# Optimization experiments

Hardware: AMD Instinct MI355X
Metric: run time of the kernel (lower is better)

## Reference

```python
import jax, jax.numpy as jnp
import numpy as np

NUM_USERS = 100000
NUM_ITEMS = 50000
EMBED_DIM = 128
NNZ = 2000000
N_LAYERS = 3


def setup_inputs() -> dict:
    key = jax.random.key(0)
    k1, k2, k3, k4, k5 = jax.random.split(key, 5)
    stdv = 1.0 / np.sqrt(EMBED_DIM)
    user_pref = jax.random.uniform(k1, (NUM_USERS, EMBED_DIM), jnp.float32, -stdv, stdv)
    item_pref = jax.random.uniform(k2, (NUM_ITEMS, EMBED_DIM), jnp.float32, -stdv, stdv)
    vals = jax.random.uniform(k3, (NNZ,), jnp.float32)
    rows = jax.random.randint(k4, (NNZ,), 0, NUM_USERS, jnp.int32)
    cols = jax.random.randint(k5, (NNZ,), 0, NUM_ITEMS, jnp.int32)
    return {"user_pref": user_pref, "item_pref": item_pref, "vals": vals,
            "rows": rows, "cols": cols}


def _spmm(vals, src_idx, dst_idx, x, num_out):
    # y[dst] += vals * x[src]  — SpMM over COO edge list
    msgs = vals[:, None] * x[src_idx]            # [nnz, D]
    return jax.ops.segment_sum(msgs, dst_idx, num_segments=num_out)


def reference(user_pref, item_pref, vals, rows, cols):
    u, it = user_pref, item_pref
    u_sum, i_sum = user_pref, item_pref
    for _ in range(N_LAYERS):
        # u_next = Graph @ item_layer ; i_next = Graph.T @ user_layer (same layer index)
        u_next = _spmm(vals, cols, rows, it, NUM_USERS)   # [U, D]
        i_next = _spmm(vals, rows, cols, u, NUM_ITEMS)    # [I, D]
        u, it = u_next, i_next
        u_sum = u_sum + u
        i_sum = i_sum + it
    inv = 1.0 / (N_LAYERS + 1)
    return (u_sum * inv, i_sum * inv)
```

## Files before the change

kernel.cpp:

```cpp
#include <hip/hip_runtime.h>


#define NUM_USERS 100000
#define NUM_ITEMS 50000
#define EMBED_DIM 128
#define NNZ_COUNT 2000000
#define NBUCK_U 391
#define NBUCK_I 196
#define EPB 8192
#define NBLK 245


__device__ __forceinline__ unsigned bf16_rnd(float f) {
    unsigned u = __float_as_uint(f);
    return (u + 0x7FFFu + ((u >> 16) & 1u)) >> 16;
}
__device__ __forceinline__ unsigned pack_bf16(float x, float y) {
    return bf16_rnd(x) | (bf16_rnd(y) << 16);
}

__global__ __launch_bounds__(256) void to_bf16_kernel(
    const float* __restrict__ a, unsigned* __restrict__ o, int n8)
{
    int i = blockIdx.x * 256 + threadIdx.x;
    if (i >= n8) return;
    const float4* a4 = reinterpret_cast<const float4*>(a);
    float4 x = a4[i * 2], y = a4[i * 2 + 1];
    uint4 r;
    r.x = pack_bf16(x.x, x.y); r.y = pack_bf16(x.z, x.w);
    r.z = pack_bf16(y.x, y.y); r.w = pack_bf16(y.z, y.w);
    reinterpret_cast<uint4*>(o)[i] = r;
}


__global__ __launch_bounds__(256) void msplit_hist(
    const int* __restrict__ rows, const int* __restrict__ cols,
    int* __restrict__ hist_u, int* __restrict__ hist_i)
{
    __shared__ int h[NBUCK_U + NBUCK_I];
    for (int i = threadIdx.x; i < NBUCK_U + NBUCK_I; i += 256) h[i] = 0;
    __syncthreads();
    const int base = blockIdx.x * EPB;
    const int end = min(base + EPB, NNZ_COUNT);
    for (int e = base + threadIdx.x; e < end; e += 256) {
        atomicAdd(&h[rows[e] >> 8], 1);
        atomicAdd(&h[NBUCK_U + (cols[e] >> 8)], 1);
    }
    __syncthreads();
    for (int b = threadIdx.x; b < NBUCK_U; b += 256)
        hist_u[b * NBLK + blockIdx.x] = h[b];
    for (int b = threadIdx.x; b < NBUCK_I; b += 256)
        hist_i[b * NBLK + blockIdx.x] = h[NBUCK_U + b];
}

__global__ __launch_bounds__(256) void msplit_offsets(
    const int* __restrict__ hist_u, const int* __restrict__ hist_i,
    int* __restrict__ offs_u, int* __restrict__ offs_i,
    int* __restrict__ tot_u, int* __restrict__ tot_i)
{
    __shared__ int buf[256];
    int b = blockIdx.x;
    const int* hist; int* offs; int* tot; int nbuck;
    if (b < NBUCK_U) { hist = hist_u; offs = offs_u; tot = tot_u; nbuck = NBUCK_U; }
    else { b -= NBUCK_U; hist = hist_i; offs = offs_i; tot = tot_i; nbuck = NBUCK_I; }
    const int t = threadIdx.x;
    const int x = (t < NBLK) ? hist[b * NBLK + t] : 0;
    buf[t] = x;
    __syncthreads();
    for (int d = 1; d < 256; d <<= 1) {
        const int y = (t >= d) ? buf[t - d] : 0;
        __syncthreads();
        buf[t] += y;
        __syncthreads();
    }
    if (t < NBLK) offs[t * nbuck + b] = buf[t] - x;
    if (t == 255) tot[b] = buf[255];
}

__global__ __launch_bounds__(512) void scan_buckets(
    const int* __restrict__ tot_u, int* __restrict__ bbase_u,
    const int* __restrict__ tot_i, int* __restrict__ bbase_i)
{
    __shared__ int buf[512];
    const int t = threadIdx.x;
    const int* tot; int* bbase; int nb;
    if (blockIdx.x == 0) { tot = tot_u; bbase = bbase_u; nb = NBUCK_U; }
    else                 { tot = tot_i; bbase = bbase_i; nb = NBUCK_I; }
    const int v = (t < nb) ? tot[t] : 0;
    buf[t] = v;
    __syncthreads();
    for (int d = 1; d < 512; d <<= 1) {
        const int y = (t >= d) ? buf[t - d] : 0;
        __syncthreads();
        buf[t] += y;
        __syncthreads();
    }
    if (t <= nb) bbase[t] = buf[t] - v;
}

__global__ __launch_bounds__(256) void msplit_scatter(
    const int* __restrict__ rows, const int* __restrict__ cols,
    const float* __restrict__ vals,
    const int* __restrict__ offs_u, const int* __restrict__ offs_i,
    const int* __restrict__ bbase_u, const int* __restrict__ bbase_i,
    int2* __restrict__ stage_u, int2* __restrict__ stage_i)
{
    __shared__ int cu[NBUCK_U];
    __shared__ int ci[NBUCK_I];
    const int t = threadIdx.x;
    for (int b = t; b < NBUCK_U; b += 256)
        cu[b] = offs_u[blockIdx.x * NBUCK_U + b] + bbase_u[b];
    for (int b = t; b < NBUCK_I; b += 256)
        ci[b] = offs_i[blockIdx.x * NBUCK_I + b] + bbase_i[b];
    __syncthreads();
    const int base = blockIdx.x * EPB;
    const int end = min(base + EPB, NNZ_COUNT);
    for (int e = base + t; e < end; e += 256) {
        const int r = rows[e];
        const int c = cols[e];
        const int vb = __float_as_int(vals[e]);
        const int su = atomicAdd(&cu[r >> 8], 1);
        stage_u[su] = make_int2(c | ((r & 255) << 16), vb);
        const int si = atomicAdd(&ci[c >> 8], 1);
        stage_i[si] = make_int2(r | ((c & 255) << 17), vb);
    }
}

__global__ __launch_bounds__(256) void bucket_build(
    const int* __restrict__ bbase_u, const int2* __restrict__ stage_u,
    int2* __restrict__ pairs_u, int* __restrict__ ptr_u,
    const int* __restrict__ bbase_i, const int2* __restrict__ stage_i,
    int2* __restrict__ pairs_i, int* __restrict__ ptr_i)
{
    __shared__ int hcnt[256];
    __shared__ int buf[256];
    __shared__ int cur[256];
    const int t = threadIdx.x;
    int b = blockIdx.x;
    const bool uside = (b < NBUCK_U);
    const int* bbase; const int2* stage; int2* pairs; int* ptr; int n; int sh;
    if (uside) { bbase = bbase_u; stage = stage_u; pairs = pairs_u; ptr = ptr_u; n = NUM_USERS; sh = 16; }
    else { b -= NBUCK_U; bbase = bbase_i; stage = stage_i; pairs = pairs_i; ptr = ptr_i; n = NUM_ITEMS; sh = 17; }
    const int beg = bbase[b];
    const int end = bbase[b + 1];

    hcnt[t] = 0;
    __syncthreads();
    for (int idx = beg + t; idx < end; idx += 256)
        atomicAdd(&hcnt[(stage[idx].x >> sh) & 255], 1);
    __syncthreads();

    const int v = hcnt[t];
    buf[t] = v;
    __syncthreads();
    for (int d = 1; d < 256; d <<= 1) {
        const int y = (t >= d) ? buf[t - d] : 0;
        __syncthreads();
        buf[t] += y;
        __syncthreads();
    }
    const int rowbase = beg + buf[t] - v;
    cur[t] = rowbase;
    const int first = b << 8;
    if (first + t < n) ptr[first + t] = rowbase;
    if (first + t == n) ptr[n] = end;
    else if (first + 256 == n && t == 0) ptr[n] = end;
    __syncthreads();

    for (int idx = beg + t; idx < end; idx += 256) {
        const int2 s = stage[idx];
        const int local   = (s.x >> sh) & 255;
        const int payload = uside ? (s.x & 0xFFFF) : (s.x & 0x1FFFF);
        const int slot = atomicAdd(&cur[local], 1);
        pairs[slot] = make_int2(payload, s.y);
    }
}


template<bool WRITE_DST, bool HAS_BASE>
__device__ __forceinline__ void spmm_row_bf(
    const int* __restrict__ ptr, const int2* __restrict__ pairs,
    const unsigned* __restrict__ src, unsigned* __restrict__ dst,
    float* __restrict__ sum, const float* __restrict__ base,
    int row, int lane, float scale)
{
    const int start = ptr[row];
    const int end   = ptr[row + 1];
    float2 acc = make_float2(0.f, 0.f);

    for (int chunk = start; chunk < end; chunk += 64) {
        const int idx = chunk + lane;
        int2 p = make_int2(0, 0);
        if (idx < end) p = pairs[idx];
        int m = end - chunk; if (m > 64) m = 64;

        int j = 0;
        for (; j + 4 <= m; j += 4) {
            const int   c0 = __shfl(p.x, j),     c1 = __shfl(p.x, j + 1);
            const int   c2 = __shfl(p.x, j + 2), c3 = __shfl(p.x, j + 3);
            const float v0 = __int_as_float(__shfl(p.y, j));
            const float v1 = __int_as_float(__shfl(p.y, j + 1));
            const float v2 = __int_as_float(__shfl(p.y, j + 2));
            const float v3 = __int_as_float(__shfl(p.y, j + 3));
            const unsigned g0 = src[(size_t)c0 * 64 + lane];
            const unsigned g1 = src[(size_t)c1 * 64 + lane];
            const unsigned g2 = src[(size_t)c2 * 64 + lane];
            const unsigned g3 = src[(size_t)c3 * 64 + lane];
            acc.x += v0 * __uint_as_float(g0 << 16);
            acc.y += v0 * __uint_as_float(g0 & 0xFFFF0000u);
            acc.x += v1 * __uint_as_float(g1 << 16);
            acc.y += v1 * __uint_as_float(g1 & 0xFFFF0000u);
            acc.x += v2 * __uint_as_float(g2 << 16);
            acc.y += v2 * __uint_as_float(g2 & 0xFFFF0000u);
            acc.x += v3 * __uint_as_float(g3 << 16);
            acc.y += v3 * __uint_as_float(g3 & 0xFFFF0000u);
        }
        for (; j < m; ++j) {
            const int   c = __shfl(p.x, j);
            const float v = __int_as_float(__shfl(p.y, j));
            const unsigned g = src[(size_t)c * 64 + lane];
            acc.x += v * __uint_as_float(g << 16);
            acc.y += v * __uint_as_float(g & 0xFFFF0000u);
        }
    }

    if (WRITE_DST) dst[(size_t)row * 64 + lane] = pack_bf16(acc.x, acc.y);

    const size_t o = (size_t)row * EMBED_DIM + (lane << 1);
    float2 bsv;
    if (HAS_BASE) bsv = *reinterpret_cast<const float2*>(base + o);
    else          bsv = *reinterpret_cast<const float2*>(sum + o);
    bsv.x = (bsv.x + acc.x) * scale;
    bsv.y = (bsv.y + acc.y) * scale;
    *reinterpret_cast<float2*>(sum + o) = bsv;
}

template<bool WRITE_DST, bool HAS_BASE>
__global__ __launch_bounds__(256) void csr_spmm_dual_bf(
    const int*  __restrict__ ptr_u, const int2* __restrict__ pairs_u,
    const unsigned* __restrict__ src_u, unsigned* __restrict__ dst_u,
    float* __restrict__ sum_u, const float* __restrict__ base_u,
    const int*  __restrict__ ptr_i, const int2* __restrict__ pairs_i,
    const unsigned* __restrict__ src_i, unsigned* __restrict__ dst_i,
    float* __restrict__ sum_i, const float* __restrict__ base_i,
    int GU, float scale)
{
    const int lane = threadIdx.x & 63;
    const int w = threadIdx.x >> 6;
    if ((int)blockIdx.x < GU) {
        const int row = blockIdx.x * 4 + w;
        if (row < NUM_USERS)
            spmm_row_bf<WRITE_DST, HAS_BASE>(ptr_u, pairs_u, src_u, dst_u, sum_u, base_u, row, lane, scale);
    } else {
        const int row = ((int)blockIdx.x - GU) * 4 + w;
        if (row < NUM_ITEMS)
            spmm_row_bf<WRITE_DST, HAS_BASE>(ptr_i, pairs_i, src_i, dst_i, sum_i, base_i, row, lane, scale);
    }
}


__global__ __launch_bounds__(256) void edge_spmm(
    const float* __restrict__ vals, const int* __restrict__ rows,
    const int* __restrict__ cols, const float* __restrict__ u_src,
    const float* __restrict__ i_src, float* __restrict__ u_dst,
    float* __restrict__ i_dst, int nnz)
{
    const int lane = threadIdx.x & 31;
    const int e = blockIdx.x * 8 + (threadIdx.x >> 5);
    if (e >= nnz) return;
    const float v = vals[e];
    const size_t ro = (size_t)rows[e] * EMBED_DIM + lane * 4;
    const size_t co = (size_t)cols[e] * EMBED_DIM + lane * 4;
    const float4 iv = *reinterpret_cast<const float4*>(i_src + co);
    const float4 uv = *reinterpret_cast<const float4*>(u_src + ro);
    atomicAdd(u_dst + ro + 0, v * iv.x); atomicAdd(u_dst + ro + 1, v * iv.y);
    atomicAdd(u_dst + ro + 2, v * iv.z); atomicAdd(u_dst + ro + 3, v * iv.w);
    atomicAdd(i_dst + co + 0, v * uv.x); atomicAdd(i_dst + co + 1, v * uv.y);
    atomicAdd(i_dst + co + 2, v * uv.z); atomicAdd(i_dst + co + 3, v * uv.w);
}

__global__ __launch_bounds__(256) void acc_scale(
    float* __restrict__ out, const float* __restrict__ x, long n, float scale)
{
    long i = ((long)blockIdx.x * blockDim.x + threadIdx.x) * 4;
    if (i >= n) return;
    float4 o = *reinterpret_cast<float4*>(out + i);
    float4 a = *reinterpret_cast<const float4*>(x + i);
    o.x = (o.x + a.x) * scale; o.y = (o.y + a.y) * scale;
    o.z = (o.z + a.z) * scale; o.w = (o.w + a.w) * scale;
    *reinterpret_cast<float4*>(out + i) = o;
}


extern "C" void kernel_launch(void* const* d_in, const int* in_sizes, int n_in,
                              void* d_out, int out_size, void* d_ws, size_t ws_size,
                              hipStream_t stream)
{
    const float* user = (const float*)d_in[0];
    const float* item = (const float*)d_in[1];
    const float* vals = (const float*)d_in[2];
    const int*   rows = (const int*)d_in[3];
    const int*   cols = (const int*)d_in[4];

    const size_t UD = (size_t)NUM_USERS * EMBED_DIM;
    const size_t ID = (size_t)NUM_ITEMS * EMBED_DIM;

    float* out_u = (float*)d_out;
    float* out_i = out_u + UD;

    char* ws = (char*)d_ws;
    unsigned* user_bf = (unsigned*)ws;              ws += UD * 2;
    unsigned* item_bf = (unsigned*)ws;              ws += ID * 2;
    unsigned* uA = (unsigned*)ws;                   ws += UD * 2;
    unsigned* uB = (unsigned*)ws;                   ws += UD * 2;
    unsigned* iA = (unsigned*)ws;                   ws += ID * 2;
    unsigned* iB = (unsigned*)ws;                   ws += ID * 2;
    int2* pairs_u = (int2*)ws;                      ws += (size_t)NNZ_COUNT * 8;
    int2* pairs_i = (int2*)ws;                      ws += (size_t)NNZ_COUNT * 8;
    int2* stage_u = (int2*)ws;                      ws += (size_t)NNZ_COUNT * 8;
    int2* stage_i = (int2*)ws;                      ws += (size_t)NNZ_COUNT * 8;
    int* ptr_u = (int*)ws;                          ws += (NUM_USERS + 1) * 4;
    int* ptr_i = (int*)ws;                          ws += (NUM_ITEMS + 1) * 4;
    int* bbase_u = (int*)ws;                        ws += (NBUCK_U + 1) * 4;
    int* bbase_i = (int*)ws;                        ws += (NBUCK_I + 1) * 4;
    const size_t REQ = (size_t)(ws - (char*)d_ws);

    int* hist_u = (int*)pairs_u;
    int* hist_i = hist_u + NBUCK_U * NBLK;
    int* offs_u = hist_i + NBUCK_I * NBLK;
    int* offs_i = offs_u + NBLK * NBUCK_U;
    int* tot_u  = offs_i + NBLK * NBUCK_I;
    int* tot_i  = tot_u + NBUCK_U;

    if (ws_size >= REQ) {
        to_bf16_kernel<<<(int)(UD / 8 / 256), 256, 0, stream>>>(user, user_bf, (int)(UD / 8));
        to_bf16_kernel<<<(int)(ID / 8 / 256), 256, 0, stream>>>(item, item_bf, (int)(ID / 8));

        msplit_hist<<<NBLK, 256, 0, stream>>>(rows, cols, hist_u, hist_i);
        msplit_offsets<<<NBUCK_U + NBUCK_I, 256, 0, stream>>>(
            hist_u, hist_i, offs_u, offs_i, tot_u, tot_i);
        scan_buckets<<<2, 512, 0, stream>>>(tot_u, bbase_u, tot_i, bbase_i);
        msplit_scatter<<<NBLK, 256, 0, stream>>>(
            rows, cols, vals, offs_u, offs_i, bbase_u, bbase_i, stage_u, stage_i);
        bucket_build<<<NBUCK_U + NBUCK_I, 256, 0, stream>>>(
            bbase_u, stage_u, pairs_u, ptr_u,
            bbase_i, stage_i, pairs_i, ptr_i);

        const int GU = (NUM_USERS + 3) / 4;
        const int GI = (NUM_ITEMS + 3) / 4;

        csr_spmm_dual_bf<true, true><<<GU + GI, 256, 0, stream>>>(
            ptr_u, pairs_u, item_bf, uA, out_u, user,
            ptr_i, pairs_i, user_bf, iA, out_i, item, GU, 1.0f);
        csr_spmm_dual_bf<true, false><<<GU + GI, 256, 0, stream>>>(
            ptr_u, pairs_u, iA, uB, out_u, nullptr,
            ptr_i, pairs_i, uA, iB, out_i, nullptr, GU, 1.0f);
        csr_spmm_dual_bf<false, false><<<GU + GI, 256, 0, stream>>>(
            ptr_u, pairs_u, iB, uA, out_u, nullptr,
            ptr_i, pairs_i, uB, iA, out_i, nullptr, GU, 0.25f);
    } else {
        char* fw = (char*)d_ws;
        float* fuA = (float*)fw;                    fw += UD * 4;
        float* fuB = (float*)fw;                    fw += UD * 4;
        float* fiA = (float*)fw;                    fw += ID * 4;
        float* fiB = (float*)fw;                    fw += ID * 4;

        const int EDGE_BLOCKS = (NNZ_COUNT + 7) / 8;
        const int ACC_U = (int)(UD / 1024), ACC_I = (int)(ID / 1024);

        hipMemcpyAsync(out_u, user, UD * 4, hipMemcpyDeviceToDevice, stream);
        hipMemcpyAsync(out_i, item, ID * 4, hipMemcpyDeviceToDevice, stream);

        hipMemsetAsync(fuA, 0, UD * 4, stream);
        hipMemsetAsync(fiA, 0, ID * 4, stream);
        edge_spmm<<<EDGE_BLOCKS, 256, 0, stream>>>(vals, rows, cols, user, item, fuA, fiA, NNZ_COUNT);
        acc_scale<<<ACC_U, 256, 0, stream>>>(out_u, fuA, (long)UD, 1.0f);
        acc_scale<<<ACC_I, 256, 0, stream>>>(out_i, fiA, (long)ID, 1.0f);

        hipMemsetAsync(fuB, 0, UD * 4, stream);
        hipMemsetAsync(fiB, 0, ID * 4, stream);
        edge_spmm<<<EDGE_BLOCKS, 256, 0, stream>>>(vals, rows, cols, fuA, fiA, fuB, fiB, NNZ_COUNT);
        acc_scale<<<ACC_U, 256, 0, stream>>>(out_u, fuB, (long)UD, 1.0f);
        acc_scale<<<ACC_I, 256, 0, stream>>>(out_i, fiB, (long)ID, 1.0f);

        hipMemsetAsync(fuA, 0, UD * 4, stream);
        hipMemsetAsync(fiA, 0, ID * 4, stream);
        edge_spmm<<<EDGE_BLOCKS, 256, 0, stream>>>(vals, rows, cols, fuB, fiB, fuA, fiA, NNZ_COUNT);
        acc_scale<<<ACC_U, 256, 0, stream>>>(out_u, fuA, (long)UD, 0.25f);
        acc_scale<<<ACC_I, 256, 0, stream>>>(out_i, fiA, (long)ID, 0.25f);
    }
}
```

Before: 704.2 us.

## Pack CSR pairs into 32-bit words and defer layer-sum accumulation to final pass

```diff
diff --git a/kernel.cpp b/kernel.cpp
--- a/kernel.cpp
+++ b/kernel.cpp
@@ -19,17 +19,26 @@
     return bf16_rnd(x) | (bf16_rnd(y) << 16);
 }
 
-__global__ __launch_bounds__(256) void to_bf16_kernel(
-    const float* __restrict__ a, unsigned* __restrict__ o, int n8)
+__global__ __launch_bounds__(256) void to_bf16_dual(
+    const float* __restrict__ a, unsigned* __restrict__ oa, int na8,
+    const float* __restrict__ b, unsigned* __restrict__ ob, int nb8)
 {
     int i = blockIdx.x * 256 + threadIdx.x;
-    if (i >= n8) return;
-    const float4* a4 = reinterpret_cast<const float4*>(a);
-    float4 x = a4[i * 2], y = a4[i * 2 + 1];
+    const float4* s4; uint4* d4;
+    if (i < na8) {
+        s4 = reinterpret_cast<const float4*>(a) + i * 2;
+        d4 = reinterpret_cast<uint4*>(oa) + i;
+    } else {
+        i -= na8;
+        if (i >= nb8) return;
+        s4 = reinterpret_cast<const float4*>(b) + i * 2;
+        d4 = reinterpret_cast<uint4*>(ob) + i;
+    }
+    float4 x = s4[0], y = s4[1];
     uint4 r;
     r.x = pack_bf16(x.x, x.y); r.y = pack_bf16(x.z, x.w);
     r.z = pack_bf16(y.x, y.y); r.w = pack_bf16(y.z, y.w);
-    reinterpret_cast<uint4*>(o)[i] = r;
+    *d4 = r;
 }
 
 
@@ -128,9 +137,9 @@
 
 __global__ __launch_bounds__(256) void bucket_build(
     const int* __restrict__ bbase_u, const int2* __restrict__ stage_u,
-    int2* __restrict__ pairs_u, int* __restrict__ ptr_u,
+    unsigned* __restrict__ pairs_u, int* __restrict__ ptr_u,
     const int* __restrict__ bbase_i, const int2* __restrict__ stage_i,
-    int2* __restrict__ pairs_i, int* __restrict__ ptr_i)
+    unsigned* __restrict__ pairs_i, int* __restrict__ ptr_i)
 {
     __shared__ int hcnt[256];
     __shared__ int buf[256];
@@ -138,7 +147,7 @@
     const int t = threadIdx.x;
     int b = blockIdx.x;
     const bool uside = (b < NBUCK_U);
-    const int* bbase; const int2* stage; int2* pairs; int* ptr; int n; int sh;
+    const int* bbase; const int2* stage; unsigned* pairs; int* ptr; int n; int sh;
     if (uside) { bbase = bbase_u; stage = stage_u; pairs = pairs_u; ptr = ptr_u; n = NUM_USERS; sh = 16; }
     else { b -= NBUCK_U; bbase = bbase_i; stage = stage_i; pairs = pairs_i; ptr = ptr_i; n = NUM_ITEMS; sh = 17; }
     const int beg = bbase[b];
@@ -169,20 +178,30 @@
 
     for (int idx = beg + t; idx < end; idx += 256) {
         const int2 s = stage[idx];
-        const int local   = (s.x >> sh) & 255;
-        const int payload = uside ? (s.x & 0xFFFF) : (s.x & 0x1FFFF);
+        const int local = (s.x >> sh) & 255;
+        const unsigned vb = bf16_rnd(__int_as_float(s.y));
+        unsigned packed;
+        if (uside) packed = (unsigned)(s.x & 0xFFFF) | (vb << 16);
+        else       packed = (unsigned)(s.x & 0x1FFFF) | ((vb & 0x7FFFu) << 17);
         const int slot = atomicAdd(&cur[local], 1);
-        pairs[slot] = make_int2(payload, s.y);
-    }
-}
-
-
-template<bool WRITE_DST, bool HAS_BASE>
+        pairs[slot] = packed;
+    }
+}
+
+
+template<bool USIDE>
+__device__ __forceinline__ void decode_pair(unsigned s, int& c, float& v) {
+    if (USIDE) { c = (int)(s & 0xFFFFu);  v = __uint_as_float(s & 0xFFFF0000u); }
+    else       { c = (int)(s & 0x1FFFFu); v = __uint_as_float((s & 0xFFFE0000u) >> 1); }
+}
+
+template<int MODE, bool USIDE>
 __device__ __forceinline__ void spmm_row_bf(
-    const int* __restrict__ ptr, const int2* __restrict__ pairs,
+    const int* __restrict__ ptr, const unsigned* __restrict__ pairs,
     const unsigned* __restrict__ src, unsigned* __restrict__ dst,
-    float* __restrict__ sum, const float* __restrict__ base,
-    int row, int lane, float scale)
+    const unsigned* __restrict__ l1, const unsigned* __restrict__ l2,
+    const float* __restrict__ base, float* __restrict__ out,
+    int row, int lane)
 {
     const int start = ptr[row];
     const int end   = ptr[row + 1];
@@ -190,71 +209,71 @@
 
     for (int chunk = start; chunk < end; chunk += 64) {
         const int idx = chunk + lane;
-        int2 p = make_int2(0, 0);
-        if (idx < end) p = pairs[idx];
+        const unsigned p = (idx < end) ? pairs[idx] : 0u;
         int m = end - chunk; if (m > 64) m = 64;
 
         int j = 0;
-        for (; j + 4 <= m; j += 4) {
-            const int   c0 = __shfl(p.x, j),     c1 = __shfl(p.x, j + 1);
-            const int   c2 = __shfl(p.x, j + 2), c3 = __shfl(p.x, j + 3);
-            const float v0 = __int_as_float(__shfl(p.y, j));
-            const float v1 = __int_as_float(__shfl(p.y, j + 1));
-            const float v2 = __int_as_float(__shfl(p.y, j + 2));
-            const float v3 = __int_as_float(__shfl(p.y, j + 3));
-            const unsigned g0 = src[(size_t)c0 * 64 + lane];
-            const unsigned g1 = src[(size_t)c1 * 64 + lane];
-            const unsigned g2 = src[(size_t)c2 * 64 + lane];
-            const unsigned g3 = src[(size_t)c3 * 64 + lane];
-            acc.x += v0 * __uint_as_float(g0 << 16);
-            acc.y += v0 * __uint_as_float(g0 & 0xFFFF0000u);
-            acc.x += v1 * __uint_as_float(g1 << 16);
-            acc.y += v1 * __uint_as_float(g1 & 0xFFFF0000u);
-            acc.x += v2 * __uint_as_float(g2 << 16);
-            acc.y += v2 * __uint_as_float(g2 & 0xFFFF0000u);
-            acc.x += v3 * __uint_as_float(g3 << 16);
-            acc.y += v3 * __uint_as_float(g3 & 0xFFFF0000u);
+        for (; j + 8 <= m; j += 8) {
+            unsigned sv[8]; int c[8]; float v[8]; unsigned g[8];
+            #pragma unroll
+            for (int k = 0; k < 8; ++k) sv[k] = (unsigned)__shfl((int)p, j + k);
+            #pragma unroll
+            for (int k = 0; k < 8; ++k) {
+                decode_pair<USIDE>(sv[k], c[k], v[k]);
+                g[k] = src[(size_t)c[k] * 64 + lane];
+            }
+            #pragma unroll
+            for (int k = 0; k < 8; ++k) {
+                acc.x += v[k] * __uint_as_float(g[k] << 16);
+                acc.y += v[k] * __uint_as_float(g[k] & 0xFFFF0000u);
+            }
         }
         for (; j < m; ++j) {
-            const int   c = __shfl(p.x, j);
-            const float v = __int_as_float(__shfl(p.y, j));
+            const unsigned s = (unsigned)__shfl((int)p, j);
+            int c; float v;
+            decode_pair<USIDE>(s, c, v);
             const unsigned g = src[(size_t)c * 64 + lane];
             acc.x += v * __uint_as_float(g << 16);
             acc.y += v * __uint_as_float(g & 0xFFFF0000u);
         }
     }
 
-    if (WRITE_DST) dst[(size_t)row * 64 + lane] = pack_bf16(acc.x, acc.y);
-
-    const size_t o = (size_t)row * EMBED_DIM + (lane << 1);
-    float2 bsv;
-    if (HAS_BASE) bsv = *reinterpret_cast<const float2*>(base + o);
-    else          bsv = *reinterpret_cast<const float2*>(sum + o);
-    bsv.x = (bsv.x + acc.x) * scale;
-    bsv.y = (bsv.y + acc.y) * scale;
-    *reinterpret_cast<float2*>(sum + o) = bsv;
-}
-
-template<bool WRITE_DST, bool HAS_BASE>
+    if (MODE == 0) {
+        dst[(size_t)row * 64 + lane] = pack_bf16(acc.x, acc.y);
+    } else {
+        const unsigned a1 = l1[(size_t)row * 64 + lane];
+        const unsigned a2 = l2[(size_t)row * 64 + lane];
+        const size_t o = (size_t)row * EMBED_DIM + (lane << 1);
+        const float2 bs = *reinterpret_cast<const float2*>(base + o);
+        float2 r;
+        r.x = (bs.x + __uint_as_float(a1 << 16) + __uint_as_float(a2 << 16) + acc.x) * 0.25f;
+        r.y = (bs.y + __uint_as_float(a1 & 0xFFFF0000u) + __uint_as_float(a2 & 0xFFFF0000u) + acc.y) * 0.25f;
+        *reinterpret_cast<float2*>(out + o) = r;
+    }
+}
+
+template<int MODE>
 __global__ __launch_bounds__(256) void csr_spmm_dual_bf(
-    const int*  __restrict__ ptr_u, const int2* __restrict__ pairs_u,
+    const int* __restrict__ ptr_u, const unsigned* __restrict__ pairs_u,
     const unsigned* __restrict__ src_u, unsigned* __restrict__ dst_u,
-    float* __restrict__ sum_u, const float* __restrict__ base_u,
-    const int*  __restrict__ ptr_i, const int2* __restrict__ pairs_i,
+    const unsigned* __restrict__ l1_u, const unsigned* __restrict__ l2_u,
+    const float* __restrict__ base_u, float* __restrict__ out_u,
+    const int* __restrict__ ptr_i, const unsigned* __restrict__ pairs_i,
     const unsigned* __restrict__ src_i, unsigned* __restrict__ dst_i,
-    float* __restrict__ sum_i, const float* __restrict__ base_i,
-    int GU, float scale)
+    const unsigned* __restrict__ l1_i, const unsigned* __restrict__ l2_i,
+    const float* __restrict__ base_i, float* __restrict__ out_i,
+    int GU)
 {
     const int lane = threadIdx.x & 63;
     const int w = threadIdx.x >> 6;
     if ((int)blockIdx.x < GU) {
         const int row = blockIdx.x * 4 + w;
         if (row < NUM_USERS)
-            spmm_row_bf<WRITE_DST, HAS_BASE>(ptr_u, pairs_u, src_u, dst_u, sum_u, base_u, row, lane, scale);
+            spmm_row_bf<MODE, true>(ptr_u, pairs_u, src_u, dst_u, l1_u, l2_u, base_u, out_u, row, lane);
     } else {
         const int row = ((int)blockIdx.x - GU) * 4 + w;
         if (row < NUM_ITEMS)
-            spmm_row_bf<WRITE_DST, HAS_BASE>(ptr_i, pairs_i, src_i, dst_i, sum_i, base_i, row, lane, scale);
+            spmm_row_bf<MODE, false>(ptr_i, pairs_i, src_i, dst_i, l1_i, l2_i, base_i, out_i, row, lane);
     }
 }
 
@@ -315,8 +334,8 @@
     unsigned* uB = (unsigned*)ws;                   ws += UD * 2;
     unsigned* iA = (unsigned*)ws;                   ws += ID * 2;
     unsigned* iB = (unsigned*)ws;                   ws += ID * 2;
-    int2* pairs_u = (int2*)ws;                      ws += (size_t)NNZ_COUNT * 8;
-    int2* pairs_i = (int2*)ws;                      ws += (size_t)NNZ_COUNT * 8;
+    unsigned* pairs_u = (unsigned*)ws;              ws += (size_t)NNZ_COUNT * 4;
+    unsigned* pairs_i = (unsigned*)ws;              ws += (size_t)NNZ_COUNT * 4;
     int2* stage_u = (int2*)ws;                      ws += (size_t)NNZ_COUNT * 8;
     int2* stage_i = (int2*)ws;                      ws += (size_t)NNZ_COUNT * 8;
     int* ptr_u = (int*)ws;                          ws += (NUM_USERS + 1) * 4;
@@ -333,8 +352,9 @@
     int* tot_i  = tot_u + NBUCK_U;
 
     if (ws_size >= REQ) {
-        to_bf16_kernel<<<(int)(UD / 8 / 256), 256, 0, stream>>>(user, user_bf, (int)(UD / 8));
-        to_bf16_kernel<<<(int)(ID / 8 / 256), 256, 0, stream>>>(item, item_bf, (int)(ID / 8));
+        const int NA8 = (int)(UD / 8), NB8 = (int)(ID / 8);
+        to_bf16_dual<<<(NA8 + NB8 + 255) / 256, 256, 0, stream>>>(
+            user, user_bf, NA8, item, item_bf, NB8);
 
         msplit_hist<<<NBLK, 256, 0, stream>>>(rows, cols, hist_u, hist_i);
         msplit_offsets<<<NBUCK_U + NBUCK_I, 256, 0, stream>>>(
@@ -349,15 +369,15 @@
         const int GU = (NUM_USERS + 3) / 4;
         const int GI = (NUM_ITEMS + 3) / 4;
 
-        csr_spmm_dual_bf<true, true><<<GU + GI, 256, 0, stream>>>(
-            ptr_u, pairs_u, item_bf, uA, out_u, user,
-            ptr_i, pairs_i, user_bf, iA, out_i, item, GU, 1.0f);
-        csr_spmm_dual_bf<true, false><<<GU + GI, 256, 0, stream>>>(
-            ptr_u, pairs_u, iA, uB, out_u, nullptr,
-            ptr_i, pairs_i, uA, iB, out_i, nullptr, GU, 1.0f);
-        csr_spmm_dual_bf<false, false><<<GU + GI, 256, 0, stream>>>(
-            ptr_u, pairs_u, iB, uA, out_u, nullptr,
-            ptr_i, pairs_i, uB, iA, out_i, nullptr, GU, 0.25f);
+        csr_spmm_dual_bf<0><<<GU + GI, 256, 0, stream>>>(
+            ptr_u, pairs_u, item_bf, uA, nullptr, nullptr, nullptr, nullptr,
+            ptr_i, pairs_i, user_bf, iA, nullptr, nullptr, nullptr, nullptr, GU);
+        csr_spmm_dual_bf<0><<<GU + GI, 256, 0, stream>>>(
+            ptr_u, pairs_u, iA, uB, nullptr, nullptr, nullptr, nullptr,
+            ptr_i, pairs_i, uA, iB, nullptr, nullptr, nullptr, nullptr, GU);
+        csr_spmm_dual_bf<1><<<GU + GI, 256, 0, stream>>>(
+            ptr_u, pairs_u, iB, nullptr, uA, uB, user, out_u,
+            ptr_i, pairs_i, uB, nullptr, iA, iB, item, out_i, GU);
     } else {
         char* fw = (char*)d_ws;
         float* fuA = (float*)fw;                    fw += UD * 4;
```

Result: faster. 657.7 us (-6.6%).
